# Performance work log

Measured on AMD Instinct MI355X. Metric: run time of the kernel, lower is better.

The kernel has to match this reference:

```python
import jax, jax.numpy as jnp
import numpy as np

B, N, M, E, D = 32, 50000, 50000, 1600000, 32


def setup_inputs() -> dict:
    key = jax.random.key(0)
    k1, k2, k3 = jax.random.split(key, 3)
    # COO indices: row 0 = src (in [0,N)), row 1 = dst (in [0,M)); N == M here
    indices = jax.random.randint(k1, (2, E), 0, N, dtype=jnp.int64)
    std = (2.0 / D) ** 0.5  # Kaiming init since d was provided
    values = jax.random.normal(k2, (E,), dtype=jnp.float32) * std
    bias = jnp.zeros((M, 1), dtype=jnp.float32)
    x = jax.random.normal(k3, (B, N, 1), dtype=jnp.float32)
    return {"x": x, "values": values, "bias": bias, "indices": indices}


def reference(x, values, bias, indices):
    # x: (B, N, 1); values: (E,); bias: (M, 1); indices: (2, E)
    src = indices[0]
    dst = indices[1]
    # gather x at src per edge and scale: (B, E)
    contrib = values[None, :] * x[:, src, 0]
    # scatter-add into dst nodes per batch element: (B, M)
    out = jax.vmap(lambda c: jax.ops.segment_sum(c, dst, num_segments=M))(contrib)
    out = out + bias[:, 0][None, :]
    return out[..., None]  # (B, M, 1)
```

## Files before the change

### kernel.cpp

```cpp
#include <hip/hip_runtime.h>


#define BATCH 32
#define DPB   128
#define NB_MAX 400
#define BIN_TPB 1024
#define BIN_CHUNK 4096
#define BIN_EPT 4
#define CAP   5120

__global__ void k_zero_i32(int* __restrict__ p, int n) {
    const int i = blockIdx.x * blockDim.x + threadIdx.x;
    if (i < n) p[i] = 0;
}

__global__ void k_tx_count(const float* __restrict__ x, float* __restrict__ xt, int N,
                           const int* __restrict__ idx, int E,
                           int* __restrict__ gcount, int NB, int TB) {
    __shared__ float tile[32][33];
    const int tx = threadIdx.x;
    const int ty = threadIdx.y;
    const int tid = ty * 32 + tx;
    if (blockIdx.x >= TB) {
        __shared__ int hist[NB_MAX];
        for (int i = tid; i < NB; i += 256) hist[i] = 0;
        __syncthreads();
        const int cb = blockIdx.x - TB;
        const int CB = gridDim.x - TB;
        const int stride = CB * 256;
        for (int e = cb * 256 + tid; e < E; e += stride) {
            atomicAdd(&hist[idx[E + e] >> 7], 1);
        }
        __syncthreads();
        for (int i = tid; i < NB; i += 256) {
            if (hist[i]) atomicAdd(&gcount[i], hist[i]);
        }
        return;
    }
    const int n0 = blockIdx.x * 32;
    #pragma unroll
    for (int k = 0; k < 4; ++k) {
        const int b = ty + 8 * k;
        const int n = n0 + tx;
        tile[tx][b] = (n < N) ? x[(size_t)b * N + n] : 0.0f;
    }
    __syncthreads();
    #pragma unroll
    for (int k = 0; k < 4; ++k) {
        const int n = n0 + ty + 8 * k;
        if (n < N) xt[(size_t)n * BATCH + tx] = tile[ty + 8 * k][tx];
    }
}

__global__ __launch_bounds__(1024) void k_scan_buckets(const int* __restrict__ gcount,
                                                       int* __restrict__ bucket_base,
                                                       int* __restrict__ gcursor,
                                                       int NB, int E) {
    __shared__ int s[1024];
    const int tid = threadIdx.x;
    const int v = (tid < NB) ? gcount[tid] : 0;
    s[tid] = v;
    __syncthreads();
    for (int off = 1; off < 1024; off <<= 1) {
        const int t = (tid >= off) ? s[tid - off] : 0;
        __syncthreads();
        s[tid] += t;
        __syncthreads();
    }
    if (tid < NB) {
        const int excl = s[tid] - v;
        bucket_base[tid] = excl;
        gcursor[tid] = excl;
    }
    if (tid == 0) bucket_base[NB] = E;
}

__global__ __launch_bounds__(BIN_TPB) void k_bin(const int* __restrict__ idx,
                                                 const float* __restrict__ values,
                                                 int* __restrict__ gcursor,
                                                 int2* __restrict__ sv,
                                                 int E, int NB) {
    __shared__ int  hist[NB_MAX];
    __shared__ int  loff[NB_MAX];
    __shared__ int  gbase[NB_MAX];
    __shared__ int2 svl[BIN_CHUNK];
    __shared__ int  gidx[BIN_CHUNK];
    const int tid = threadIdx.x;
    if (tid < NB) hist[tid] = 0;
    __syncthreads();

    const int c0 = blockIdx.x * BIN_CHUNK;
    const int nE = min(BIN_CHUNK, E - c0);
    int d[BIN_EPT];
    #pragma unroll
    for (int i = 0; i < BIN_EPT; ++i) {
        const int e = c0 + tid + i * BIN_TPB;
        d[i] = (e < E) ? idx[E + e] : -1;
        if (d[i] >= 0) atomicAdd(&hist[d[i] >> 7], 1);
    }
    __syncthreads();
    if (tid < 64) {
        int carry = 0;
        for (int c = 0; c < NB; c += 64) {
            const int j = c + tid;
            const int v = (j < NB) ? hist[j] : 0;
            int inc = v;
            #pragma unroll
            for (int dlt = 1; dlt < 64; dlt <<= 1) {
                const int t = __shfl_up(inc, dlt, 64);
                if (tid >= dlt) inc += t;
            }
            if (j < NB) loff[j] = carry + inc - v;
            carry += __shfl(inc, 63, 64);
        }
    }
    __syncthreads();
    if (tid < NB) {
        const int c = hist[tid];
        gbase[tid] = c ? atomicAdd(&gcursor[tid], c) : 0;
        hist[tid] = 0;
    }
    __syncthreads();
    #pragma unroll
    for (int i = 0; i < BIN_EPT; ++i) {
        if (d[i] >= 0) {
            const int e = c0 + tid + i * BIN_TPB;
            const int bkt = d[i] >> 7;
            const int off = atomicAdd(&hist[bkt], 1);
            const int slot = loff[bkt] + off;
            const int packed = (idx[e] & 0xFFFF) | ((d[i] & 127) << 16);
            svl[slot]  = make_int2(packed, __float_as_int(values[e]));
            gidx[slot] = gbase[bkt] + off;
        }
    }
    __syncthreads();
    for (int s = tid; s < nE; s += BIN_TPB) {
        sv[gidx[s]] = svl[s];
    }
}

__global__ __launch_bounds__(1024) void k_sort_gather(const int2* __restrict__ sv,
                                                      const int* __restrict__ bbase,
                                                      const float* __restrict__ xt,
                                                      const float* __restrict__ bias,
                                                      float* __restrict__ out, int M) {
    __shared__ int2 stage[CAP];
    __shared__ unsigned short perm[CAP];
    __shared__ int cnt[DPB];
    __shared__ int off[DPB + 1];
    __shared__ int cur[DPB];
    __shared__ float tile[DPB][33];

    const int bkt = blockIdx.x;
    const int beg = bbase[bkt];
    const int end = bbase[bkt + 1];
    const int tid = threadIdx.x;
    const int w    = tid >> 6;
    const int lane = tid & 63;
    const int g    = lane >> 3;
    const int j    = lane & 7;
    const int m0   = bkt * DPB;
    const float4* __restrict__ xt4 = (const float4*)xt;

    for (int i = tid; i < DPB * 33; i += 1024) ((float*)tile)[i] = 0.0f;

    for (int t0 = beg; t0 < end; t0 += CAP) {
        const int nE = min(CAP, end - t0);
        __syncthreads();
        if (tid < DPB) cnt[tid] = 0;
        __syncthreads();
        for (int i = tid; i < nE; i += 1024) {
            const int2 a = sv[t0 + i];
            stage[i] = a;
            atomicAdd(&cnt[(a.x >> 16) & 127], 1);
        }
        __syncthreads();
        if (tid < 64) {
            int carry = 0;
            #pragma unroll
            for (int c = 0; c < DPB; c += 64) {
                const int jj = c + tid;
                const int v = cnt[jj];
                int inc = v;
                #pragma unroll
                for (int dlt = 1; dlt < 64; dlt <<= 1) {
                    const int t = __shfl_up(inc, dlt, 64);
                    if (tid >= dlt) inc += t;
                }
                off[jj] = carry + inc - v;
                cur[jj] = carry + inc - v;
                carry += __shfl(inc, 63, 64);
            }
            if (tid == 0) off[DPB] = carry;
        }
        __syncthreads();
        for (int i = tid; i < nE; i += 1024) {
            const int dl = (stage[i].x >> 16) & 127;
            const int p = atomicAdd(&cur[dl], 1);
            perm[p] = (unsigned short)i;
        }
        __syncthreads();
        #pragma unroll
        for (int k = 0; k < DPB / 16; ++k) {
            const int r  = w + 16 * k;
            const int rb = off[r];
            const int re = off[r + 1];
            float ax = 0.f, ay = 0.f, az = 0.f, aw_ = 0.f;
            float bx = 0.f, by = 0.f, bz = 0.f, bw = 0.f;
            int q = rb;
            for (; q + 15 < re; q += 16) {
                const int2 eA = stage[perm[q + g]];
                const int2 eB = stage[perm[q + 8 + g]];
                const float4 xA = xt4[(size_t)(eA.x & 0xFFFF) * 8 + j];
                const float4 xB = xt4[(size_t)(eB.x & 0xFFFF) * 8 + j];
                const float vA = __int_as_float(eA.y);
                const float vB = __int_as_float(eB.y);
                ax += vA * xA.x; ay += vA * xA.y; az += vA * xA.z; aw_ += vA * xA.w;
                bx += vB * xB.x; by += vB * xB.y; bz += vB * xB.z; bw  += vB * xB.w;
            }
            for (; q < re; q += 8) {
                if (q + g < re) {
                    const int2 e = stage[perm[q + g]];
                    const float4 xv = xt4[(size_t)(e.x & 0xFFFF) * 8 + j];
                    const float v = __int_as_float(e.y);
                    ax += v * xv.x; ay += v * xv.y; az += v * xv.z; aw_ += v * xv.w;
                }
            }
            ax += bx; ay += by; az += bz; aw_ += bw;
            #pragma unroll
            for (int d = 8; d < 64; d <<= 1) {
                ax  += __shfl_xor(ax, d, 64);
                ay  += __shfl_xor(ay, d, 64);
                az  += __shfl_xor(az, d, 64);
                aw_ += __shfl_xor(aw_, d, 64);
            }
            if (g == 0) {
                tile[r][j * 4 + 0] += ax;
                tile[r][j * 4 + 1] += ay;
                tile[r][j * 4 + 2] += az;
                tile[r][j * 4 + 3] += aw_;
            }
        }
    }
    __syncthreads();
    for (int i = tid; i < 32 * DPB; i += 1024) {
        const int b = i >> 7;
        const int c = i & 127;
        const int m2 = m0 + c;
        if (m2 < M) out[(size_t)b * M + m2] = tile[c][b] + bias[m2];
    }
}

__global__ void k_init_out_t(const float* __restrict__ bias, float* __restrict__ out_t, int M) {
    const int i = blockIdx.x * blockDim.x + threadIdx.x;
    if (i < M * BATCH) out_t[i] = bias[i >> 5];
}

__global__ void k_scatter(const float* __restrict__ xt, const float* __restrict__ values,
                          const int* __restrict__ idx, float* __restrict__ out_t, int E) {
    const int t = blockIdx.x * blockDim.x + threadIdx.x;
    const int e = t >> 5;
    const int b = t & 31;
    if (e < E) {
        const int src = idx[e];
        const int dst = idx[E + e];
        const float contrib = values[e] * xt[(size_t)src * BATCH + b];
        atomicAdd(&out_t[(size_t)dst * BATCH + b], contrib);
    }
}

__global__ void k_transpose_out(const float* __restrict__ out_t, float* __restrict__ out, int M) {
    __shared__ float tile[32][33];
    const int m0 = blockIdx.x * 32;
    const int tx = threadIdx.x;
    const int ty = threadIdx.y;
    #pragma unroll
    for (int k = 0; k < 4; ++k) {
        const int m = m0 + ty + 8 * k;
        if (m < M) tile[ty + 8 * k][tx] = out_t[(size_t)m * BATCH + tx];
    }
    __syncthreads();
    #pragma unroll
    for (int k = 0; k < 4; ++k) {
        const int b = ty + 8 * k;
        const int m = m0 + tx;
        if (m < M) out[(size_t)b * M + m] = tile[tx][b];
    }
}

extern "C" void kernel_launch(void* const* d_in, const int* in_sizes, int n_in,
                              void* d_out, int out_size, void* d_ws, size_t ws_size,
                              hipStream_t stream) {
    const float* x      = (const float*)d_in[0];
    const float* values = (const float*)d_in[1];
    const float* bias   = (const float*)d_in[2];
    const int*   idx    = (const int*)d_in[3];

    const int N = in_sizes[0] / BATCH;
    const int E = in_sizes[3] / 2;
    const int M = in_sizes[2];
    const int NB = (M + DPB - 1) / DPB;

    float* out = (float*)d_out;

    char* base = (char*)d_ws;
    size_t off = 0;
    auto carve = [&](size_t bytes) -> void* {
        void* r = base + off;
        off = (off + bytes + 511) & ~(size_t)511;
        return r;
    };
    float* xt      = (float*)carve((size_t)N * BATCH * sizeof(float));
    float* out_t   = (float*)carve((size_t)M * BATCH * sizeof(float));
    int2*  sv      = (int2*)carve((size_t)E * sizeof(int2));
    int*   gcount  = (int*)carve((size_t)NB * sizeof(int));
    int*   bbase   = (int*)carve((size_t)(NB + 1) * sizeof(int));
    int*   gcursor = (int*)carve((size_t)NB * sizeof(int));
    const size_t csr_needed = off;

    dim3 tblk(32, 8);
    const int TB = (N + 31) / 32;

    const bool use_csr = (csr_needed <= ws_size) && (N <= 65536) && (M <= 65536)
                         && (NB <= NB_MAX);
    if (use_csr) {
        k_zero_i32<<<(NB + 255) / 256, 256, 0, stream>>>(gcount, NB);
        k_tx_count<<<TB + 512, tblk, 0, stream>>>(x, xt, N, idx, E, gcount, NB, TB);
        k_scan_buckets<<<1, 1024, 0, stream>>>(gcount, bbase, gcursor, NB, E);
        k_bin<<<(E + BIN_CHUNK - 1) / BIN_CHUNK, BIN_TPB, 0, stream>>>(idx, values, gcursor, sv, E, NB);
        k_sort_gather<<<NB, 1024, 0, stream>>>(sv, bbase, xt, bias, out, M);
    } else {
        k_tx_count<<<TB, tblk, 0, stream>>>(x, xt, N, idx, E, gcount, NB, TB);
        k_init_out_t<<<(M * BATCH + 255) / 256, 256, 0, stream>>>(bias, out_t, M);
        const long long total = (long long)E * BATCH;
        k_scatter<<<(int)((total + 255) / 256), 256, 0, stream>>>(xt, values, idx, out_t, E);
        k_transpose_out<<<(M + 31) / 32, tblk, 0, stream>>>(out_t, out, M);
    }
}
```

Baseline: 135.8 us.

## Fold bucket scan into bin and gather kernels, vectorize index and output accesses

Drops the separate single-block scan kernel. Each k_bin and k_sort_gather block now recomputes the bucket prefix sum from gcount in shared memory, and gcursor becomes a relative cursor zeroed together with gcount. It also switches the dst-index histogram, the edge loads in k_bin, the sv staging loads and the output stores to 128-bit vector accesses. This saves one kernel launch and serialization point and reduces memory transactions, at the cost of a redundant per-block scan of about 400 entries.

```diff
diff --git a/kernel.cpp b/kernel.cpp
--- a/kernel.cpp
+++ b/kernel.cpp
@@ -6,7 +6,6 @@
 #define NB_MAX 400
 #define BIN_TPB 1024
 #define BIN_CHUNK 4096
-#define BIN_EPT 4
 #define CAP   5120
 
 __global__ void k_zero_i32(int* __restrict__ p, int n) {
@@ -28,8 +27,20 @@
         const int cb = blockIdx.x - TB;
         const int CB = gridDim.x - TB;
         const int stride = CB * 256;
-        for (int e = cb * 256 + tid; e < E; e += stride) {
-            atomicAdd(&hist[idx[E + e] >> 7], 1);
+        if ((E & 3) == 0) {
+            const int4* __restrict__ dst4 = (const int4*)(idx + E);
+            const int P = E >> 2;
+            for (int p = cb * 256 + tid; p < P; p += stride) {
+                const int4 d4 = dst4[p];
+                atomicAdd(&hist[d4.x >> 7], 1);
+                atomicAdd(&hist[d4.y >> 7], 1);
+                atomicAdd(&hist[d4.z >> 7], 1);
+                atomicAdd(&hist[d4.w >> 7], 1);
+            }
+        } else {
+            for (int e = cb * 256 + tid; e < E; e += stride) {
+                atomicAdd(&hist[idx[E + e] >> 7], 1);
+            }
         }
         __syncthreads();
         for (int i = tid; i < NB; i += 256) {
@@ -52,34 +63,13 @@
     }
 }
 
-__global__ __launch_bounds__(1024) void k_scan_buckets(const int* __restrict__ gcount,
-                                                       int* __restrict__ bucket_base,
-                                                       int* __restrict__ gcursor,
-                                                       int NB, int E) {
-    __shared__ int s[1024];
-    const int tid = threadIdx.x;
-    const int v = (tid < NB) ? gcount[tid] : 0;
-    s[tid] = v;
-    __syncthreads();
-    for (int off = 1; off < 1024; off <<= 1) {
-        const int t = (tid >= off) ? s[tid - off] : 0;
-        __syncthreads();
-        s[tid] += t;
-        __syncthreads();
-    }
-    if (tid < NB) {
-        const int excl = s[tid] - v;
-        bucket_base[tid] = excl;
-        gcursor[tid] = excl;
-    }
-    if (tid == 0) bucket_base[NB] = E;
-}
-
 __global__ __launch_bounds__(BIN_TPB) void k_bin(const int* __restrict__ idx,
                                                  const float* __restrict__ values,
+                                                 const int* __restrict__ gcount,
                                                  int* __restrict__ gcursor,
                                                  int2* __restrict__ sv,
                                                  int E, int NB) {
+    __shared__ int  bb[NB_MAX + 1];
     __shared__ int  hist[NB_MAX];
     __shared__ int  loff[NB_MAX];
     __shared__ int  gbase[NB_MAX];
@@ -87,17 +77,38 @@
     __shared__ int  gidx[BIN_CHUNK];
     const int tid = threadIdx.x;
     if (tid < NB) hist[tid] = 0;
+    if (tid < 64) {
+        int carry = 0;
+        for (int c = 0; c < NB; c += 64) {
+            const int j = c + tid;
+            const int v = (j < NB) ? gcount[j] : 0;
+            int inc = v;
+            #pragma unroll
+            for (int dlt = 1; dlt < 64; dlt <<= 1) {
+                const int t = __shfl_up(inc, dlt, 64);
+                if (tid >= dlt) inc += t;
+            }
+            if (j < NB) bb[j] = carry + inc - v;
+            carry += __shfl(inc, 63, 64);
+        }
+        if (tid == 0) bb[NB] = carry;
+    }
     __syncthreads();
 
     const int c0 = blockIdx.x * BIN_CHUNK;
     const int nE = min(BIN_CHUNK, E - c0);
-    int d[BIN_EPT];
-    #pragma unroll
-    for (int i = 0; i < BIN_EPT; ++i) {
-        const int e = c0 + tid + i * BIN_TPB;
-        d[i] = (e < E) ? idx[E + e] : -1;
-        if (d[i] >= 0) atomicAdd(&hist[d[i] >> 7], 1);
-    }
+    const int e0 = c0 + (tid << 2);
+    const bool v4 = ((E & 3) == 0) && (e0 + 3 < E);
+    int d[4] = {-1, -1, -1, -1};
+    if (v4) {
+        const int4 d4 = *(const int4*)(idx + E + e0);
+        d[0] = d4.x; d[1] = d4.y; d[2] = d4.z; d[3] = d4.w;
+    } else {
+        #pragma unroll
+        for (int k = 0; k < 4; ++k) if (e0 + k < E) d[k] = idx[E + e0 + k];
+    }
+    #pragma unroll
+    for (int k = 0; k < 4; ++k) if (d[k] >= 0) atomicAdd(&hist[d[k] >> 7], 1);
     __syncthreads();
     if (tid < 64) {
         int carry = 0;
@@ -117,43 +128,56 @@
     __syncthreads();
     if (tid < NB) {
         const int c = hist[tid];
-        gbase[tid] = c ? atomicAdd(&gcursor[tid], c) : 0;
+        gbase[tid] = c ? (bb[tid] + atomicAdd(&gcursor[tid], c)) : 0;
         hist[tid] = 0;
     }
     __syncthreads();
-    #pragma unroll
-    for (int i = 0; i < BIN_EPT; ++i) {
-        if (d[i] >= 0) {
-            const int e = c0 + tid + i * BIN_TPB;
-            const int bkt = d[i] >> 7;
+    int   s[4];
+    float vv[4];
+    if (v4) {
+        const int4   s4 = *(const int4*)(idx + e0);
+        const float4 v4v = *(const float4*)(values + e0);
+        s[0] = s4.x; s[1] = s4.y; s[2] = s4.z; s[3] = s4.w;
+        vv[0] = v4v.x; vv[1] = v4v.y; vv[2] = v4v.z; vv[3] = v4v.w;
+    } else {
+        #pragma unroll
+        for (int k = 0; k < 4; ++k) {
+            if (e0 + k < E) { s[k] = idx[e0 + k]; vv[k] = values[e0 + k]; }
+            else { s[k] = 0; vv[k] = 0.0f; }
+        }
+    }
+    #pragma unroll
+    for (int k = 0; k < 4; ++k) {
+        if (d[k] >= 0) {
+            const int bkt = d[k] >> 7;
             const int off = atomicAdd(&hist[bkt], 1);
             const int slot = loff[bkt] + off;
-            const int packed = (idx[e] & 0xFFFF) | ((d[i] & 127) << 16);
-            svl[slot]  = make_int2(packed, __float_as_int(values[e]));
+            const int packed = (s[k] & 0xFFFF) | ((d[k] & 127) << 16);
+            svl[slot]  = make_int2(packed, __float_as_int(vv[k]));
             gidx[slot] = gbase[bkt] + off;
         }
     }
     __syncthreads();
-    for (int s = tid; s < nE; s += BIN_TPB) {
-        sv[gidx[s]] = svl[s];
+    for (int q = tid; q < nE; q += BIN_TPB) {
+        sv[gidx[q]] = svl[q];
     }
 }
 
 __global__ __launch_bounds__(1024) void k_sort_gather(const int2* __restrict__ sv,
-                                                      const int* __restrict__ bbase,
+                                                      const int* __restrict__ gcount,
                                                       const float* __restrict__ xt,
                                                       const float* __restrict__ bias,
-                                                      float* __restrict__ out, int M) {
+                                                      float* __restrict__ out,
+                                                      int M, int NB) {
     __shared__ int2 stage[CAP];
     __shared__ unsigned short perm[CAP];
+    __shared__ int bbs[NB_MAX + 1];
     __shared__ int cnt[DPB];
     __shared__ int off[DPB + 1];
     __shared__ int cur[DPB];
     __shared__ float tile[DPB][33];
 
     const int bkt = blockIdx.x;
-    const int beg = bbase[bkt];
-    const int end = bbase[bkt + 1];
     const int tid = threadIdx.x;
     const int w    = tid >> 6;
     const int lane = tid & 63;
@@ -162,16 +186,52 @@
     const int m0   = bkt * DPB;
     const float4* __restrict__ xt4 = (const float4*)xt;
 
+    if (tid < 64) {
+        int carry = 0;
+        for (int c = 0; c < NB; c += 64) {
+            const int jj = c + tid;
+            const int v = (jj < NB) ? gcount[jj] : 0;
+            int inc = v;
+            #pragma unroll
+            for (int dlt = 1; dlt < 64; dlt <<= 1) {
+                const int t = __shfl_up(inc, dlt, 64);
+                if (tid >= dlt) inc += t;
+            }
+            if (jj < NB) bbs[jj] = carry + inc - v;
+            carry += __shfl(inc, 63, 64);
+        }
+        if (tid == 0) bbs[NB] = carry;
+    }
     for (int i = tid; i < DPB * 33; i += 1024) ((float*)tile)[i] = 0.0f;
+    __syncthreads();
+    const int beg = bbs[bkt];
+    const int end = bbs[bkt + 1];
 
     for (int t0 = beg; t0 < end; t0 += CAP) {
         const int nE = min(CAP, end - t0);
         __syncthreads();
         if (tid < DPB) cnt[tid] = 0;
         __syncthreads();
-        for (int i = tid; i < nE; i += 1024) {
-            const int2 a = sv[t0 + i];
-            stage[i] = a;
+        const int head = (t0 & 1);
+        if (head && tid == 0) {
+            const int2 a = sv[t0];
+            stage[0] = a;
+            atomicAdd(&cnt[(a.x >> 16) & 127], 1);
+        }
+        const int npair = (nE - head) >> 1;
+        const int4* __restrict__ sv4 = (const int4*)(sv + t0 + head);
+        for (int p = tid; p < npair; p += 1024) {
+            const int4 q = sv4[p];
+            const int i0 = head + (p << 1);
+            stage[i0]     = make_int2(q.x, q.y);
+            stage[i0 + 1] = make_int2(q.z, q.w);
+            atomicAdd(&cnt[(q.x >> 16) & 127], 1);
+            atomicAdd(&cnt[(q.z >> 16) & 127], 1);
+        }
+        if (((nE - head) & 1) && tid == 1023) {
+            const int i0 = head + (npair << 1);
+            const int2 a = sv[t0 + i0];
+            stage[i0] = a;
             atomicAdd(&cnt[(a.x >> 16) & 127], 1);
         }
         __syncthreads();
@@ -243,11 +303,36 @@
         }
     }
     __syncthreads();
-    for (int i = tid; i < 32 * DPB; i += 1024) {
-        const int b = i >> 7;
-        const int c = i & 127;
-        const int m2 = m0 + c;
-        if (m2 < M) out[(size_t)b * M + m2] = tile[c][b] + bias[m2];
+    if ((M & 3) == 0) {
+        float4* __restrict__ out4 = (float4*)out;
+        const float4* __restrict__ bias4 = (const float4*)bias;
+        for (int i = tid; i < 32 * (DPB / 4); i += 1024) {
+            const int b  = i >> 5;
+            const int c4 = i & 31;
+            const int m2 = m0 + (c4 << 2);
+            if (m2 + 3 < M) {
+                const float4 bv = bias4[(m0 >> 2) + c4];
+                float4 o;
+                o.x = tile[c4 * 4 + 0][b] + bv.x;
+                o.y = tile[c4 * 4 + 1][b] + bv.y;
+                o.z = tile[c4 * 4 + 2][b] + bv.z;
+                o.w = tile[c4 * 4 + 3][b] + bv.w;
+                out4[((size_t)b * M + m2) >> 2] = o;
+            } else {
+                #pragma unroll
+                for (int k = 0; k < 4; ++k) {
+                    const int m3 = m2 + k;
+                    if (m3 < M) out[(size_t)b * M + m3] = tile[c4 * 4 + k][b] + bias[m3];
+                }
+            }
+        }
+    } else {
+        for (int i = tid; i < 32 * DPB; i += 1024) {
+            const int b = i >> 7;
+            const int c = i & 127;
+            const int m2 = m0 + c;
+            if (m2 < M) out[(size_t)b * M + m2] = tile[c][b] + bias[m2];
+        }
     }
 }
 
@@ -313,10 +398,10 @@
     float* xt      = (float*)carve((size_t)N * BATCH * sizeof(float));
     float* out_t   = (float*)carve((size_t)M * BATCH * sizeof(float));
     int2*  sv      = (int2*)carve((size_t)E * sizeof(int2));
-    int*   gcount  = (int*)carve((size_t)NB * sizeof(int));
-    int*   bbase   = (int*)carve((size_t)(NB + 1) * sizeof(int));
-    int*   gcursor = (int*)carve((size_t)NB * sizeof(int));
+    int*   gz      = (int*)carve((size_t)2 * NB * sizeof(int));
     const size_t csr_needed = off;
+    int* gcount  = gz;
+    int* gcursor = gz + NB;
 
     dim3 tblk(32, 8);
     const int TB = (N + 31) / 32;
@@ -324,11 +409,10 @@
     const bool use_csr = (csr_needed <= ws_size) && (N <= 65536) && (M <= 65536)
                          && (NB <= NB_MAX);
     if (use_csr) {
-        k_zero_i32<<<(NB + 255) / 256, 256, 0, stream>>>(gcount, NB);
+        k_zero_i32<<<(2 * NB + 255) / 256, 256, 0, stream>>>(gz, 2 * NB);
         k_tx_count<<<TB + 512, tblk, 0, stream>>>(x, xt, N, idx, E, gcount, NB, TB);
-        k_scan_buckets<<<1, 1024, 0, stream>>>(gcount, bbase, gcursor, NB, E);
-        k_bin<<<(E + BIN_CHUNK - 1) / BIN_CHUNK, BIN_TPB, 0, stream>>>(idx, values, gcursor, sv, E, NB);
-        k_sort_gather<<<NB, 1024, 0, stream>>>(sv, bbase, xt, bias, out, M);
+        k_bin<<<(E + BIN_CHUNK - 1) / BIN_CHUNK, BIN_TPB, 0, stream>>>(idx, values, gcount, gcursor, sv, E, NB);
+        k_sort_gather<<<NB, 1024, 0, stream>>>(sv, gcount, xt, bias, out, M, NB);
     } else {
         k_tx_count<<<TB, tblk, 0, stream>>>(x, xt, N, idx, E, gcount, NB, TB);
         k_init_out_t<<<(M * BATCH + 255) / 256, 256, 0, stream>>>(bias, out_t, M);
```

Measured after the change: 137.9 us. Within noise of the previous version (+1.6%).
